# Kernel tuning notes

Measured on AMD Instinct MI355X. Metric: run time of the kernel, lower is better.

The kernel has to match this reference:

```python
import jax, jax.numpy as jnp
import numpy as np

E = 8      # number of parts/experts
H = 128    # hidden width
D_IN = 3   # xyz coords
D_OUT = 1  # occupancy


def setup_inputs() -> dict:
    key = jax.random.key(0)
    ks = jax.random.split(key, 9)
    coords = jax.random.normal(ks[0], (1, 65536, D_IN), dtype=jnp.float32)
    s = 0.05
    return {
        "coords": coords,
        "W0": jax.random.normal(ks[1], (E, H, D_IN), dtype=jnp.float32) * s,
        "b0": jax.random.normal(ks[2], (E, H), dtype=jnp.float32) * s,
        "W1": jax.random.normal(ks[3], (E, H, H), dtype=jnp.float32) * s,
        "b1": jax.random.normal(ks[4], (E, H), dtype=jnp.float32) * s,
        "W2": jax.random.normal(ks[5], (E, H, H), dtype=jnp.float32) * s,
        "b2": jax.random.normal(ks[6], (E, H), dtype=jnp.float32) * s,
        "Wo": jax.random.normal(ks[7], (E, D_OUT, H), dtype=jnp.float32) * s,
        "bo": jax.random.normal(ks[8], (E, D_OUT), dtype=jnp.float32) * s,
    }


def reference(coords, W0, b0, W1, b1, W2, b2, Wo, bo):
    # Batched (grouped) MLP over experts: equivalent to vmap(functional_call)
    # over stacked per-part parameters in the torch module.
    # coords: [B, N, 3]; weights: [E, out, in]
    h = jax.nn.relu(jnp.einsum('bnd,ehd->ebnh', coords, W0) + b0[:, None, None, :])
    h = jax.nn.relu(jnp.einsum('ebnh,egh->ebng', h, W1) + b1[:, None, None, :])
    h = jax.nn.relu(jnp.einsum('ebnh,egh->ebng', h, W2) + b2[:, None, None, :])
    expert_out = jnp.einsum('ebnh,eoh->ebno', h, Wo) + bo[:, None, None, :]  # [E,B,N,1]
    max_occ = jnp.max(expert_out, axis=0)  # combine experts via max, [B,N,1]
    return max_occ
```

## Files before the change

### kernel.cpp

```cpp
#include <hip/hip_runtime.h>

#define NE 8
#define HD 128
#define NPTS 65536
#define TM 64

typedef __bf16 bf16x8 __attribute__((ext_vector_type(8)));
typedef __bf16 bf16x4 __attribute__((ext_vector_type(4)));
typedef float f32x4 __attribute__((ext_vector_type(4)));

__device__ __forceinline__ unsigned int f2bf(float f) {
    unsigned int u = __float_as_uint(f);
    u += 0x7FFFu + ((u >> 16) & 1u);
    return u >> 16;
}

__device__ __forceinline__ unsigned int swz(int row, int byte_in_row) {
    return (unsigned int)((row * 256 + byte_in_row) ^ ((row & 7) << 4));
}

__device__ __forceinline__ void bar_lds() {
    asm volatile("s_waitcnt lgkmcnt(0)\ns_barrier" ::: "memory");
}

template<int KB0, int KB1>
__device__ __forceinline__ void loadA128(const unsigned short* __restrict__ Ag,
                                         bf16x8 (&a)[2][4], int tc, int lr, int lg) {
#pragma unroll
    for (int ca = 0; ca < 2; ++ca)
#pragma unroll
        for (int kb = KB0; kb < KB1; ++kb)
            a[ca][kb] = *(const bf16x8*)(Ag + (tc + ca * 16 + lr) * HD + kb * 32 + lg * 8);
}

__device__ __forceinline__ void loadA32(const unsigned short* __restrict__ Ag,
                                        bf16x8 (&a)[2][1], int tc, int lr, int lg) {
#pragma unroll
    for (int ca = 0; ca < 2; ++ca)
        a[ca][0] = *(const bf16x8*)(Ag + (tc + ca * 16 + lr) * 32 + lg * 8);
}

template<int NKB, bool BSWZ, int BSTR>
__device__ __forceinline__ void gemm_core(const bf16x8 (&a)[2][NKB], const char* Bb,
                                          f32x4 (&acc)[2][4], int lr, int lg) {
#pragma unroll
    for (int kb = 0; kb < NKB; ++kb) {
        bf16x8 b[4];
#pragma unroll
        for (int nb = 0; nb < 4; ++nb) {
            int r = nb * 16 + lr;
            int byte = kb * 64 + lg * 16;
            const char* p = BSWZ ? (Bb + swz(r, byte)) : (Bb + r * BSTR + byte);
            b[nb] = *(const bf16x8*)p;
        }
#pragma unroll
        for (int ca = 0; ca < 2; ++ca)
#pragma unroll
            for (int nb = 0; nb < 4; ++nb)
                acc[ca][nb] = __builtin_amdgcn_mfma_f32_16x16x32_bf16(a[ca][kb], b[nb], acc[ca][nb], 0, 0, 0);
    }
}

__device__ __forceinline__ void epi_store(const f32x4 (&acc)[2][4], char* Db,
                                          const float* __restrict__ bias,
                                          int tc, int lr, int lg) {
#pragma unroll
    for (int ca = 0; ca < 2; ++ca) {
        int c0 = tc + ca * 16 + lg * 4;
        float4 bs = *(const float4*)(bias + c0);
#pragma unroll
        for (int nb = 0; nb < 4; ++nb) {
            int r = nb * 16 + lr;
            bf16x4 pk;
            pk[0] = (__bf16)fmaxf(acc[ca][nb][0] + bs.x, 0.f);
            pk[1] = (__bf16)fmaxf(acc[ca][nb][1] + bs.y, 0.f);
            pk[2] = (__bf16)fmaxf(acc[ca][nb][2] + bs.z, 0.f);
            pk[3] = (__bf16)fmaxf(acc[ca][nb][3] + bs.w, 0.f);
            *(bf16x4*)(Db + swz(r, c0 * 2)) = pk;
        }
    }
}

__global__ void prep_kernel(const float* __restrict__ W0,
                            const float* __restrict__ W1,
                            const float* __restrict__ W2,
                            unsigned int* __restrict__ W1b,
                            unsigned int* __restrict__ W2b,
                            unsigned int* __restrict__ W0p) {
    int i = blockIdx.x * 256 + threadIdx.x;
    float2 v = *(const float2*)(W1 + 2 * i);
    W1b[i] = f2bf(v.x) | (f2bf(v.y) << 16);
    float2 u = *(const float2*)(W2 + 2 * i);
    W2b[i] = f2bf(u.x) | (f2bf(u.y) << 16);
    if (i < NE * HD * 16) {
        int row = i >> 4;
        int kk = (i & 15) * 2;
        float a = (kk < 3) ? W0[row * 3 + kk] : 0.f;
        float b = (kk + 1 < 3) ? W0[row * 3 + kk + 1] : 0.f;
        W0p[i] = f2bf(a) | (f2bf(b) << 16);
    }
}

#define XPS 40

__global__ __launch_bounds__(256, 4) void moe_main(
    const float* __restrict__ coords,
    const float* __restrict__ b0, const float* __restrict__ b1,
    const float* __restrict__ b2,
    const float* __restrict__ Wo, const float* __restrict__ bo,
    const unsigned short* __restrict__ W0p,
    const unsigned short* __restrict__ W1b,
    const unsigned short* __restrict__ W2b,
    float* __restrict__ out) {
    __shared__ __align__(16) unsigned short hA[TM * HD];
    __shared__ __align__(16) unsigned short hB[TM * HD];
    __shared__ __align__(16) unsigned short Xp[TM * XPS];
    __shared__ __align__(16) float part[NE * TM];

    const int tid = threadIdx.x;
    const int lane = tid & 63;
    const int w = tid >> 6;
    const int lr = lane & 15;
    const int lg = lane >> 4;
    const int tc = w * 32;
    const int row0 = blockIdx.x * TM;

    if (tid < TM) {
        unsigned int* rowp = (unsigned int*)(Xp + tid * XPS);
        float c0 = coords[(row0 + tid) * 3 + 0];
        float c1 = coords[(row0 + tid) * 3 + 1];
        float c2 = coords[(row0 + tid) * 3 + 2];
        rowp[0] = f2bf(c0) | (f2bf(c1) << 16);
        rowp[1] = f2bf(c2);
#pragma unroll
        for (int i = 2; i < XPS / 2; ++i) rowp[i] = 0;
    } else if (tid >= 128) {
        ((float4*)part)[tid - 128] = (float4){0.f, 0.f, 0.f, 0.f};
    }
    bar_lds();

    bf16x8 a0[2][1], a1[2][4], a2[2][4];
    loadA32(W0p, a0, tc, lr, lg);
    loadA128<0, 2>(W1b, a1, tc, lr, lg);

    for (int e = 0; e < NE; ++e) {
        const unsigned short* W1e = W1b + e * HD * HD;
        const unsigned short* W2e = W2b + e * HD * HD;
        const int e1 = (e < NE - 1) ? e + 1 : e;
        f32x4 acc[2][4];

#pragma unroll
        for (int ca = 0; ca < 2; ++ca)
#pragma unroll
            for (int nb = 0; nb < 4; ++nb) acc[ca][nb] = (f32x4){0.f, 0.f, 0.f, 0.f};
        gemm_core<1, false, XPS * 2>(a0, (const char*)Xp, acc, lr, lg);
        loadA128<2, 4>(W1e, a1, tc, lr, lg);
        epi_store(acc, (char*)hA, b0 + e * HD, tc, lr, lg);
        bar_lds();

#pragma unroll
        for (int ca = 0; ca < 2; ++ca)
#pragma unroll
            for (int nb = 0; nb < 4; ++nb) acc[ca][nb] = (f32x4){0.f, 0.f, 0.f, 0.f};
        gemm_core<4, true, 0>(a1, (const char*)hA, acc, lr, lg);
        loadA128<0, 2>(W2e, a2, tc, lr, lg);
        epi_store(acc, (char*)hB, b1 + e * HD, tc, lr, lg);
        bar_lds();

        loadA128<2, 4>(W2e, a2, tc, lr, lg);
#pragma unroll
        for (int ca = 0; ca < 2; ++ca)
#pragma unroll
            for (int nb = 0; nb < 4; ++nb) acc[ca][nb] = (f32x4){0.f, 0.f, 0.f, 0.f};
        gemm_core<4, true, 0>(a2, (const char*)hB, acc, lr, lg);
        loadA32(W0p + e1 * HD * 32, a0, tc, lr, lg);
        loadA128<0, 2>(W1b + e1 * HD * HD, a1, tc, lr, lg);

        {
            const float* b2e = b2 + e * HD;
            const float* Woe = Wo + e * HD;
            float s[4] = {0.f, 0.f, 0.f, 0.f};
#pragma unroll
            for (int ca = 0; ca < 2; ++ca) {
                int c0 = tc + ca * 16 + lg * 4;
                float4 bs = *(const float4*)(b2e + c0);
                float4 wo = *(const float4*)(Woe + c0);
#pragma unroll
                for (int nb = 0; nb < 4; ++nb) {
                    float v0 = fmaxf(acc[ca][nb][0] + bs.x, 0.f);
                    float v1 = fmaxf(acc[ca][nb][1] + bs.y, 0.f);
                    float v2 = fmaxf(acc[ca][nb][2] + bs.z, 0.f);
                    float v3 = fmaxf(acc[ca][nb][3] + bs.w, 0.f);
                    s[nb] += v0 * wo.x + v1 * wo.y + v2 * wo.z + v3 * wo.w;
                }
            }
#pragma unroll
            for (int nb = 0; nb < 4; ++nb) {
                s[nb] += __shfl_xor(s[nb], 16);
                s[nb] += __shfl_xor(s[nb], 32);
            }
            if (lg == 0) {
#pragma unroll
                for (int nb = 0; nb < 4; ++nb)
                    atomicAdd(&part[e * TM + nb * 16 + lr], s[nb]);
            }
        }
    }

    bar_lds();
    if (tid < TM) {
        float m = -3.0e38f;
#pragma unroll
        for (int e = 0; e < NE; ++e) m = fmaxf(m, part[e * TM + tid] + bo[e]);
        out[row0 + tid] = m;
    }
}

extern "C" void kernel_launch(void* const* d_in, const int* in_sizes, int n_in,
                              void* d_out, int out_size, void* d_ws, size_t ws_size,
                              hipStream_t stream) {
    const float* coords = (const float*)d_in[0];
    const float* W0 = (const float*)d_in[1];
    const float* b0 = (const float*)d_in[2];
    const float* W1 = (const float*)d_in[3];
    const float* b1 = (const float*)d_in[4];
    const float* W2 = (const float*)d_in[5];
    const float* b2 = (const float*)d_in[6];
    const float* Wo = (const float*)d_in[7];
    const float* bo = (const float*)d_in[8];
    float* out = (float*)d_out;

    char* ws = (char*)d_ws;
    unsigned short* W1b = (unsigned short*)(ws);
    unsigned short* W2b = (unsigned short*)(ws + 262144);
    unsigned short* W0p = (unsigned short*)(ws + 524288);

    prep_kernel<<<dim3(256), dim3(256), 0, stream>>>(
        W0, W1, W2, (unsigned int*)W1b, (unsigned int*)W2b, (unsigned int*)W0p);

    moe_main<<<dim3(NPTS / TM), dim3(256), 0, stream>>>(
        coords, b0, b1, b2, Wo, bo, W0p, W1b, W2b, out);
}
```

Before: 83.94 us.

## Fuse next expert's first layer into current iteration and drop atomics

The first-layer GEMM for the next expert now runs right after the current expert's last layer. This cuts the number of workgroup barriers per expert from three to two. The coordinate B-fragments are loaded from LDS into registers once and reused for every expert, and biases are prefetched earlier. Shared-memory atomicAdd accumulation is replaced by plain per-wave partial stores, with the expert max kept in a running register. In exchange, register pressure rises and the last iteration does one redundant first-layer GEMM.

```diff
diff --git a/kernel.cpp b/kernel.cpp
--- a/kernel.cpp
+++ b/kernel.cpp
@@ -34,25 +34,21 @@
 }
 
 __device__ __forceinline__ void loadA32(const unsigned short* __restrict__ Ag,
-                                        bf16x8 (&a)[2][1], int tc, int lr, int lg) {
+                                        bf16x8 (&a)[2], int tc, int lr, int lg) {
 #pragma unroll
     for (int ca = 0; ca < 2; ++ca)
-        a[ca][0] = *(const bf16x8*)(Ag + (tc + ca * 16 + lr) * 32 + lg * 8);
-}
-
-template<int NKB, bool BSWZ, int BSTR>
-__device__ __forceinline__ void gemm_core(const bf16x8 (&a)[2][NKB], const char* Bb,
+        a[ca] = *(const bf16x8*)(Ag + (tc + ca * 16 + lr) * 32 + lg * 8);
+}
+
+template<int NKB>
+__device__ __forceinline__ void gemm_core(const bf16x8 (&a)[2][4], const char* Bb,
                                           f32x4 (&acc)[2][4], int lr, int lg) {
 #pragma unroll
     for (int kb = 0; kb < NKB; ++kb) {
         bf16x8 b[4];
 #pragma unroll
-        for (int nb = 0; nb < 4; ++nb) {
-            int r = nb * 16 + lr;
-            int byte = kb * 64 + lg * 16;
-            const char* p = BSWZ ? (Bb + swz(r, byte)) : (Bb + r * BSTR + byte);
-            b[nb] = *(const bf16x8*)p;
-        }
+        for (int nb = 0; nb < 4; ++nb)
+            b[nb] = *(const bf16x8*)(Bb + swz(nb * 16 + lr, kb * 64 + lg * 16));
 #pragma unroll
         for (int ca = 0; ca < 2; ++ca)
 #pragma unroll
@@ -62,20 +58,18 @@
 }
 
 __device__ __forceinline__ void epi_store(const f32x4 (&acc)[2][4], char* Db,
-                                          const float* __restrict__ bias,
-                                          int tc, int lr, int lg) {
+                                          const float4 (&bs)[2], int tc, int lr, int lg) {
 #pragma unroll
     for (int ca = 0; ca < 2; ++ca) {
         int c0 = tc + ca * 16 + lg * 4;
-        float4 bs = *(const float4*)(bias + c0);
 #pragma unroll
         for (int nb = 0; nb < 4; ++nb) {
             int r = nb * 16 + lr;
             bf16x4 pk;
-            pk[0] = (__bf16)fmaxf(acc[ca][nb][0] + bs.x, 0.f);
-            pk[1] = (__bf16)fmaxf(acc[ca][nb][1] + bs.y, 0.f);
-            pk[2] = (__bf16)fmaxf(acc[ca][nb][2] + bs.z, 0.f);
-            pk[3] = (__bf16)fmaxf(acc[ca][nb][3] + bs.w, 0.f);
+            pk[0] = (__bf16)fmaxf(acc[ca][nb][0] + bs[ca].x, 0.f);
+            pk[1] = (__bf16)fmaxf(acc[ca][nb][1] + bs[ca].y, 0.f);
+            pk[2] = (__bf16)fmaxf(acc[ca][nb][2] + bs[ca].z, 0.f);
+            pk[3] = (__bf16)fmaxf(acc[ca][nb][3] + bs[ca].w, 0.f);
             *(bf16x4*)(Db + swz(r, c0 * 2)) = pk;
         }
     }
@@ -115,7 +109,7 @@
     __shared__ __align__(16) unsigned short hA[TM * HD];
     __shared__ __align__(16) unsigned short hB[TM * HD];
     __shared__ __align__(16) unsigned short Xp[TM * XPS];
-    __shared__ __align__(16) float part[NE * TM];
+    __shared__ __align__(16) float part[4 * TM];
 
     const int tid = threadIdx.x;
     const int lane = tid & 63;
@@ -134,66 +128,83 @@
         rowp[1] = f2bf(c2);
 #pragma unroll
         for (int i = 2; i < XPS / 2; ++i) rowp[i] = 0;
-    } else if (tid >= 128) {
-        ((float4*)part)[tid - 128] = (float4){0.f, 0.f, 0.f, 0.f};
     }
     bar_lds();
 
-    bf16x8 a0[2][1], a1[2][4], a2[2][4];
+    bf16x8 xb[4];
+#pragma unroll
+    for (int nb = 0; nb < 4; ++nb)
+        xb[nb] = *(const bf16x8*)(Xp + (nb * 16 + lr) * XPS + lg * 8);
+
+    bf16x8 a0[2], a1[2][4], a2[2][4];
     loadA32(W0p, a0, tc, lr, lg);
     loadA128<0, 2>(W1b, a1, tc, lr, lg);
 
+    {
+        float4 bs0[2];
+#pragma unroll
+        for (int ca = 0; ca < 2; ++ca) bs0[ca] = *(const float4*)(b0 + tc + ca * 16 + lg * 4);
+        f32x4 acc0[2][4];
+#pragma unroll
+        for (int ca = 0; ca < 2; ++ca)
+#pragma unroll
+            for (int nb = 0; nb < 4; ++nb) {
+                acc0[ca][nb] = (f32x4){0.f, 0.f, 0.f, 0.f};
+                acc0[ca][nb] = __builtin_amdgcn_mfma_f32_16x16x32_bf16(a0[ca], xb[nb], acc0[ca][nb], 0, 0, 0);
+            }
+        loadA32(W0p + 1 * HD * 32, a0, tc, lr, lg);
+        epi_store(acc0, (char*)hA, bs0, tc, lr, lg);
+    }
+    bar_lds();
+
+    float bmax = -3.0e38f;
+
     for (int e = 0; e < NE; ++e) {
-        const unsigned short* W1e = W1b + e * HD * HD;
         const unsigned short* W2e = W2b + e * HD * HD;
         const int e1 = (e < NE - 1) ? e + 1 : e;
+        const int e2 = (e < NE - 2) ? e + 2 : e1;
+
+        float4 bs1[2];
+#pragma unroll
+        for (int ca = 0; ca < 2; ++ca) bs1[ca] = *(const float4*)(b1 + e * HD + tc + ca * 16 + lg * 4);
+        loadA128<2, 4>(W1b + e * HD * HD, a1, tc, lr, lg);
         f32x4 acc[2][4];
-
 #pragma unroll
         for (int ca = 0; ca < 2; ++ca)
 #pragma unroll
             for (int nb = 0; nb < 4; ++nb) acc[ca][nb] = (f32x4){0.f, 0.f, 0.f, 0.f};
-        gemm_core<1, false, XPS * 2>(a0, (const char*)Xp, acc, lr, lg);
-        loadA128<2, 4>(W1e, a1, tc, lr, lg);
-        epi_store(acc, (char*)hA, b0 + e * HD, tc, lr, lg);
+        gemm_core<4>(a1, (const char*)hA, acc, lr, lg);
+        loadA128<0, 2>(W2e, a2, tc, lr, lg);
+        epi_store(acc, (char*)hB, bs1, tc, lr, lg);
         bar_lds();
 
+        float4 bs2[2], wo[2], bs0[2];
+#pragma unroll
+        for (int ca = 0; ca < 2; ++ca) {
+            int c0 = tc + ca * 16 + lg * 4;
+            bs2[ca] = *(const float4*)(b2 + e * HD + c0);
+            wo[ca] = *(const float4*)(Wo + e * HD + c0);
+            bs0[ca] = *(const float4*)(b0 + e1 * HD + c0);
+        }
+        loadA128<2, 4>(W2e, a2, tc, lr, lg);
 #pragma unroll
         for (int ca = 0; ca < 2; ++ca)
 #pragma unroll
             for (int nb = 0; nb < 4; ++nb) acc[ca][nb] = (f32x4){0.f, 0.f, 0.f, 0.f};
-        gemm_core<4, true, 0>(a1, (const char*)hA, acc, lr, lg);
-        loadA128<0, 2>(W2e, a2, tc, lr, lg);
-        epi_store(acc, (char*)hB, b1 + e * HD, tc, lr, lg);
-        bar_lds();
-
-        loadA128<2, 4>(W2e, a2, tc, lr, lg);
-#pragma unroll
-        for (int ca = 0; ca < 2; ++ca)
-#pragma unroll
-            for (int nb = 0; nb < 4; ++nb) acc[ca][nb] = (f32x4){0.f, 0.f, 0.f, 0.f};
-        gemm_core<4, true, 0>(a2, (const char*)hB, acc, lr, lg);
-        loadA32(W0p + e1 * HD * 32, a0, tc, lr, lg);
-        loadA128<0, 2>(W1b + e1 * HD * HD, a1, tc, lr, lg);
+        gemm_core<4>(a2, (const char*)hB, acc, lr, lg);
 
         {
-            const float* b2e = b2 + e * HD;
-            const float* Woe = Wo + e * HD;
             float s[4] = {0.f, 0.f, 0.f, 0.f};
 #pragma unroll
-            for (int ca = 0; ca < 2; ++ca) {
-                int c0 = tc + ca * 16 + lg * 4;
-                float4 bs = *(const float4*)(b2e + c0);
-                float4 wo = *(const float4*)(Woe + c0);
+            for (int ca = 0; ca < 2; ++ca)
 #pragma unroll
                 for (int nb = 0; nb < 4; ++nb) {
-                    float v0 = fmaxf(acc[ca][nb][0] + bs.x, 0.f);
-                    float v1 = fmaxf(acc[ca][nb][1] + bs.y, 0.f);
-                    float v2 = fmaxf(acc[ca][nb][2] + bs.z, 0.f);
-                    float v3 = fmaxf(acc[ca][nb][3] + bs.w, 0.f);
-                    s[nb] += v0 * wo.x + v1 * wo.y + v2 * wo.z + v3 * wo.w;
+                    float v0 = fmaxf(acc[ca][nb][0] + bs2[ca].x, 0.f);
+                    float v1 = fmaxf(acc[ca][nb][1] + bs2[ca].y, 0.f);
+                    float v2 = fmaxf(acc[ca][nb][2] + bs2[ca].z, 0.f);
+                    float v3 = fmaxf(acc[ca][nb][3] + bs2[ca].w, 0.f);
+                    s[nb] += v0 * wo[ca].x + v1 * wo[ca].y + v2 * wo[ca].z + v3 * wo[ca].w;
                 }
-            }
 #pragma unroll
             for (int nb = 0; nb < 4; ++nb) {
                 s[nb] += __shfl_xor(s[nb], 16);
@@ -201,19 +212,30 @@
             }
             if (lg == 0) {
 #pragma unroll
-                for (int nb = 0; nb < 4; ++nb)
-                    atomicAdd(&part[e * TM + nb * 16 + lr], s[nb]);
+                for (int nb = 0; nb < 4; ++nb) part[w * TM + nb * 16 + lr] = s[nb];
             }
         }
-    }
-
-    bar_lds();
-    if (tid < TM) {
-        float m = -3.0e38f;
-#pragma unroll
-        for (int e = 0; e < NE; ++e) m = fmaxf(m, part[e * TM + tid] + bo[e]);
-        out[row0 + tid] = m;
-    }
+
+        {
+            f32x4 acc0[2][4];
+#pragma unroll
+            for (int ca = 0; ca < 2; ++ca)
+#pragma unroll
+                for (int nb = 0; nb < 4; ++nb) {
+                    acc0[ca][nb] = (f32x4){0.f, 0.f, 0.f, 0.f};
+                    acc0[ca][nb] = __builtin_amdgcn_mfma_f32_16x16x32_bf16(a0[ca], xb[nb], acc0[ca][nb], 0, 0, 0);
+                }
+            loadA32(W0p + e2 * HD * 32, a0, tc, lr, lg);
+            loadA128<0, 2>(W1b + e1 * HD * HD, a1, tc, lr, lg);
+            epi_store(acc0, (char*)hA, bs0, tc, lr, lg);
+        }
+        bar_lds();
+
+        if (tid < TM)
+            bmax = fmaxf(bmax, part[tid] + part[TM + tid] + part[2 * TM + tid] + part[3 * TM + tid] + bo[e]);
+    }
+
+    if (tid < TM) out[row0 + tid] = bmax;
 }
 
 extern "C" void kernel_launch(void* const* d_in, const int* in_sizes, int n_in,
```

Result: slower. 110.5 us (+31.7%).
